# Kernel optimization log

Hardware: AMD Instinct MI355X
Metric: run time of the kernel (lower is better)

The kernel has to match this reference:

```python
import jax, jax.numpy as jnp
import numpy as np

B, S, D, H = 2, 2048, 128, 8  # batch, seq, num_hidden(=head dim), num_heads
EPS = 1e-5


def setup_inputs() -> dict:
    key = jax.random.key(0)
    ks = jax.random.split(key, 12)
    sc = 0.02
    return {
        "query": jax.random.normal(ks[0], (B, S, D), dtype=jnp.float32),
        "Wq": jax.random.normal(ks[1], (2 * H * D, D), dtype=jnp.float32) * sc,
        "bq": jnp.zeros((2 * H * D,), dtype=jnp.float32),
        "Wk": jax.random.normal(ks[2], (2 * H * D, D), dtype=jnp.float32) * sc,
        "bk": jnp.zeros((2 * H * D,), dtype=jnp.float32),
        "Wv": jax.random.normal(ks[3], (H * D, D), dtype=jnp.float32) * sc,
        "bv": jnp.zeros((H * D,), dtype=jnp.float32),
        "Wo": jax.random.normal(ks[4], (D, H * D), dtype=jnp.float32) * sc,
        "bo": jnp.zeros((D,), dtype=jnp.float32),
        "gn_w": jnp.ones((H,), dtype=jnp.float32),
        "gn_b": jnp.zeros((H,), dtype=jnp.float32),
        "lam": jax.random.uniform(ks[5], (), dtype=jnp.float32),
    }


def reference(query, Wq, bq, Wk, bk, Wv, bv, Wo, bo, gn_w, gn_b, lam):
    # Faithful to the torch module: the .view calls are raw reshapes (no
    # transpose), d_k=1 so scale is 1, mask=None path (no causal mask),
    # dropout in eval mode, _lambda == _lambda_init == lam.
    q = (query @ Wq.T + bq).reshape(B, H, S, 2 * D)
    k = (query @ Wk.T + bk).reshape(B, H, S, 2 * D)
    v = (query @ Wv.T + bv).reshape(B, H, S, D)
    q1, q2 = q[..., :D], q[..., D:]
    k1, k2 = k[..., :D], k[..., D:]
    s1 = jnp.einsum("bhqd,bhkd->bhqk", q1, k1)  # / sqrt(d_k=1)
    s2 = jnp.einsum("bhqd,bhkd->bhqk", q2, k2)
    attn = jax.nn.softmax(s1, axis=-1) - lam * jax.nn.softmax(s2, axis=-1)
    out = jnp.einsum("bhqk,bhkd->bhqd", attn, v)          # (B,H,S,D)
    out = out.transpose(0, 2, 1, 3).reshape(B, H, S, D)   # faithful raw reshape
    # GroupNorm(num_groups=H, num_channels=H): normalize per (b, h) over (S, D)
    mean = out.mean(axis=(2, 3), keepdims=True)
    var = out.var(axis=(2, 3), keepdims=True)
    out = (out - mean) * jax.lax.rsqrt(var + EPS)
    out = out * gn_w[None, :, None, None] + gn_b[None, :, None, None]
    out = out * (1.0 - lam)
    # torch.cat([out[:, i] for i in range(H)], dim=-1) -> (B, S, H*D)
    out = out.transpose(0, 2, 1, 3).reshape(B, S, H * D)
    return out @ Wo.T + bo
```

## Files before the change

### kernel.cpp

```cpp
#include <hip/hip_runtime.h>

typedef __bf16 bf16x8 __attribute__((ext_vector_type(8)));
typedef __bf16 bf16x4 __attribute__((ext_vector_type(4)));
typedef float  f32x4  __attribute__((ext_vector_type(4)));

#define MFMA16(a,b,c) __builtin_amdgcn_mfma_f32_16x16x32_bf16((a),(b),(c),0,0,0)

__device__ __forceinline__ bf16x8 cvt8(float4 a, float4 b) {
  bf16x8 v;
  v[0]=(__bf16)a.x; v[1]=(__bf16)a.y; v[2]=(__bf16)a.z; v[3]=(__bf16)a.w;
  v[4]=(__bf16)b.x; v[5]=(__bf16)b.y; v[6]=(__bf16)b.z; v[7]=(__bf16)b.w;
  return v;
}
__device__ __forceinline__ bf16x4 cvt4(float4 a) {
  bf16x4 v;
  v[0]=(__bf16)a.x; v[1]=(__bf16)a.y; v[2]=(__bf16)a.z; v[3]=(__bf16)a.w;
  return v;
}


__global__ void to_bf16(const float* __restrict__ q,  const float* __restrict__ wq,
                        const float* __restrict__ wk, const float* __restrict__ wv,
                        __bf16* __restrict__ qb,  __bf16* __restrict__ wqb,
                        __bf16* __restrict__ wkb, __bf16* __restrict__ wvb)
{
  const long e = (long)(blockIdx.x * 256 + threadIdx.x) * 8;
  const float* src; __bf16* dst; long off;
  if (e < 524288)       { src = q;  dst = qb;  off = e; }
  else if (e < 786432)  { src = wq; dst = wqb; off = e - 524288; }
  else if (e < 1048576) { src = wk; dst = wkb; off = e - 786432; }
  else                  { src = wv; dst = wvb; off = e - 1048576; }
  *(bf16x8*)(dst + off) = cvt8(*(const float4*)(src + off), *(const float4*)(src + off + 4));
}

#define LDA 136
__global__ __launch_bounds__(256, 2) void qkv_gemm(
    const __bf16* __restrict__ queryb,
    const __bf16* __restrict__ Wqb, const float* __restrict__ bq,
    const __bf16* __restrict__ Wkb, const float* __restrict__ bk,
    const __bf16* __restrict__ Wvb, const float* __restrict__ bv,
    __bf16* __restrict__ Qbf, __bf16* __restrict__ Kbf, __bf16* __restrict__ Vbf)
{
  __shared__ __bf16 As[128 * LDA];
  __shared__ __bf16 Bs[128 * LDA];
  const int t = threadIdx.x;
  const int tile = blockIdx.x;
  const int tm = tile / 40, tn = tile % 40;
  const int m0 = tm * 128, n0 = tn * 128;

  const __bf16* wbase; const float* bias;
  __bf16* obase; int ocol0; int ostride; float oscale;
  if (n0 < 2048)      { wbase = Wqb + n0*128;        bias = bq + n0;        obase = Qbf; ocol0 = n0;      ostride = 2048; oscale = 1.4426950408889634f; }
  else if (n0 < 4096) { wbase = Wkb + (n0-2048)*128; bias = bk + (n0-2048); obase = Kbf; ocol0 = n0-2048; ostride = 2048; oscale = 1.0f; }
  else                { wbase = Wvb + (n0-4096)*128; bias = bv + (n0-4096); obase = Vbf; ocol0 = n0-4096; ostride = 1024; oscale = 1.0f; }

  const __bf16* abase = queryb + (long)m0 * 128;
  for (int r = 0; r < 2; ++r) {
    int e = (r*256 + t) * 32;
    int row = e >> 7, col = e & 127;
    #pragma unroll
    for (int c = 0; c < 4; ++c) {
      *(bf16x8*)&As[row*LDA + col + c*8] = *(const bf16x8*)(abase + (long)row*128 + col + c*8);
      *(bf16x8*)&Bs[row*LDA + col + c*8] = *(const bf16x8*)(wbase + (long)row*128 + col + c*8);
    }
  }
  __syncthreads();

  const int w = t >> 6, lane = t & 63;
  const int lo = lane & 15, quad = lane >> 4;
  const int wm = w >> 1, wn = w & 1;

  f32x4 acc[4][4];
  #pragma unroll
  for (int i = 0; i < 4; ++i)
    #pragma unroll
    for (int j = 0; j < 4; ++j) acc[i][j] = (f32x4){0.f,0.f,0.f,0.f};

  #pragma unroll
  for (int ks = 0; ks < 4; ++ks) {
    bf16x8 af[4], bfr[4];
    #pragma unroll
    for (int i = 0; i < 4; ++i)
      af[i] = *(const bf16x8*)&As[(wm*64 + i*16 + lo)*LDA + ks*32 + quad*8];
    #pragma unroll
    for (int j = 0; j < 4; ++j)
      bfr[j] = *(const bf16x8*)&Bs[(wn*64 + j*16 + lo)*LDA + ks*32 + quad*8];
    #pragma unroll
    for (int i = 0; i < 4; ++i)
      #pragma unroll
      for (int j = 0; j < 4; ++j)
        acc[i][j] = MFMA16(bfr[j], af[i], acc[i][j]);
  }
  #pragma unroll
  for (int j = 0; j < 4; ++j) {
    const int colb = ocol0 + wn*64 + j*16 + quad*4;
    const f32x4 b4 = *(const f32x4*)(bias + wn*64 + j*16 + quad*4);
    #pragma unroll
    for (int i = 0; i < 4; ++i) {
      const int row = m0 + wm*64 + i*16 + lo;
      bf16x4 v;
      #pragma unroll
      for (int r = 0; r < 4; ++r) v[r] = (__bf16)((acc[i][j][r] + b4[r]) * oscale);
      *(bf16x4*)&obase[(long)row*ostride + colb] = v;
    }
  }
}

__global__ void v_transpose(const __bf16* __restrict__ Vbf, __bf16* __restrict__ Vt)
{
  __shared__ __bf16 tile[128 * 136];
  const int t = threadIdx.x;
  const int bh = blockIdx.x >> 4, st = blockIdx.x & 15;
  const __bf16* src = Vbf + (long)bh*262144 + st*16384;
  for (int r = 0; r < 8; ++r) {
    int e = (r*256 + t) * 8;
    int row = e >> 7, col = e & 127;
    *(bf16x8*)&tile[row*136 + col] = *(const bf16x8*)(src + row*128 + col);
  }
  __syncthreads();
  __bf16* dst = Vt + (long)bh*262144 + st*128;
  for (int r = 0; r < 8; ++r) {
    int e = (r*256 + t) * 8;
    int d = e >> 7, s2c = e & 127;
    bf16x8 v;
    #pragma unroll
    for (int i = 0; i < 8; ++i) v[i] = tile[(s2c + i)*136 + d];
    *(bf16x8*)(dst + d*2048 + s2c) = v;
  }
}

#define LDK 264
#define LDV 40
__global__ __launch_bounds__(256, 2) void attn(
    const __bf16* __restrict__ Qbf, const __bf16* __restrict__ Kbf,
    const __bf16* __restrict__ Vt, float* __restrict__ O,
    const float* __restrict__ lam_p, float* __restrict__ stats)
{
  __shared__ __bf16 Ks[2][32 * LDK];
  __shared__ __bf16 Vs[2][128 * LDV];
  __shared__ float red[8];
  const int t = threadIdx.x;
  const int w = t >> 6, lane = t & 63;
  const int lo = lane & 15, quad = lane >> 4;
  const int s = w & 1, qg = w >> 1;
  const int bh = blockIdx.x & 15, qb = blockIdx.x >> 4;
  const float lam = *lam_p;

  const __bf16* Qh = Qbf + (long)bh*524288;
  const __bf16* Kh = Kbf + (long)bh*524288;
  const __bf16* Vh = Vt  + (long)bh*262144;
  const int qrow0 = qb*64 + qg*32;

  bf16x8 qf[2][4];
  #pragma unroll
  for (int qt = 0; qt < 2; ++qt)
    #pragma unroll
    for (int ks = 0; ks < 4; ++ks)
      qf[qt][ks] = *(const bf16x8*)(Qh + (long)(qrow0 + qt*16 + lo)*256 + s*128 + ks*32 + quad*8);

  int ke[2], ksrow[2], kcol[2], vdd[2], vch[2];
  #pragma unroll
  for (int r = 0; r < 2; ++r) {
    ke[r] = (r*256 + t) * 16;
    const int row = ke[r] >> 8;
    kcol[r] = ke[r] & 255;
    ksrow[r] = (row & 3) + ((row >> 2) & 1)*16 + ((row >> 3) & 3)*4;
    const int c = r*256 + t;
    vdd[r] = c >> 2; vch[r] = c & 3;
  }

  bf16x8 kra[2][2], vra[2];
  #pragma unroll
  for (int r = 0; r < 2; ++r) {
    kra[r][0] = *(const bf16x8*)(Kh + ke[r]);
    kra[r][1] = *(const bf16x8*)(Kh + ke[r] + 8);
    vra[r]    = *(const bf16x8*)(Vh + (long)vdd[r]*2048 + vch[r]*8);
  }
  #pragma unroll
  for (int r = 0; r < 2; ++r) {
    *(bf16x8*)&Ks[0][ksrow[r]*LDK + kcol[r]]     = kra[r][0];
    *(bf16x8*)&Ks[0][ksrow[r]*LDK + kcol[r] + 8] = kra[r][1];
    *(bf16x8*)&Vs[0][vdd[r]*LDV + vch[r]*8]      = vra[r];
  }

  f32x4 acc[2][8];
  #pragma unroll
  for (int qt = 0; qt < 2; ++qt)
    #pragma unroll
    for (int mt = 0; mt < 8; ++mt) acc[qt][mt] = (f32x4){0.f,0.f,0.f,0.f};
  float lsum[2] = {0.f, 0.f};

  for (int kt = 0; kt < 64; ++kt) {
    __syncthreads();
    if (kt + 1 < 64) {
      #pragma unroll
      for (int r = 0; r < 2; ++r) {
        kra[r][0] = *(const bf16x8*)(Kh + (long)(kt+1)*8192 + ke[r]);
        kra[r][1] = *(const bf16x8*)(Kh + (long)(kt+1)*8192 + ke[r] + 8);
        vra[r]    = *(const bf16x8*)(Vh + (long)vdd[r]*2048 + (kt+1)*32 + vch[r]*8);
      }
    }
    const __bf16* kb = Ks[kt & 1];
    const __bf16* vb = Vs[kt & 1];

    f32x4 sf[2][2];
    #pragma unroll
    for (int qt = 0; qt < 2; ++qt)
      #pragma unroll
      for (int nt = 0; nt < 2; ++nt) sf[qt][nt] = (f32x4){0.f,0.f,0.f,0.f};
    #pragma unroll
    for (int nt = 0; nt < 2; ++nt) {
      const int krow = lo + nt*16;
      #pragma unroll
      for (int ks = 0; ks < 4; ++ks) {
        bf16x8 kf = *(const bf16x8*)&kb[krow*LDK + s*128 + ks*32 + quad*8];
        sf[0][nt] = MFMA16(kf, qf[0][ks], sf[0][nt]);
        sf[1][nt] = MFMA16(kf, qf[1][ks], sf[1][nt]);
      }
    }

    bf16x8 pf[2];
    #pragma unroll
    for (int qt = 0; qt < 2; ++qt) {
      #pragma unroll
      for (int nt = 0; nt < 2; ++nt) {
        #pragma unroll
        for (int r = 0; r < 4; ++r) {
          float p = __builtin_exp2f(sf[qt][nt][r]);
          lsum[qt] += p;
          pf[qt][nt*4+r] = (__bf16)p;
        }
      }
    }

    #pragma unroll
    for (int mt = 0; mt < 8; ++mt) {
      bf16x8 vf = *(const bf16x8*)&vb[(mt*16 + lo)*LDV + quad*8];
      acc[0][mt] = MFMA16(vf, pf[0], acc[0][mt]);
      acc[1][mt] = MFMA16(vf, pf[1], acc[1][mt]);
    }

    if (kt + 1 < 64) {
      __bf16* kn = Ks[(kt+1) & 1];
      __bf16* vn = Vs[(kt+1) & 1];
      #pragma unroll
      for (int r = 0; r < 2; ++r) {
        *(bf16x8*)&kn[ksrow[r]*LDK + kcol[r]]     = kra[r][0];
        *(bf16x8*)&kn[ksrow[r]*LDK + kcol[r] + 8] = kra[r][1];
        *(bf16x8*)&vn[vdd[r]*LDV + vch[r]*8]      = vra[r];
      }
    }
  }

  #pragma unroll
  for (int qt = 0; qt < 2; ++qt) {
    lsum[qt] += __shfl_xor(lsum[qt], 16);
    lsum[qt] += __shfl_xor(lsum[qt], 32);
  }
  float inv[2];
  const float nume = (s == 0) ? 1.f : lam;
  inv[0] = nume / lsum[0];
  inv[1] = nume / lsum[1];

  float* fs = (float*)Ks;
  __syncthreads();
  if (s == 1) {
    #pragma unroll
    for (int qt = 0; qt < 2; ++qt)
      #pragma unroll
      for (int mt = 0; mt < 8; ++mt) {
        f32x4 o;
        #pragma unroll
        for (int r = 0; r < 4; ++r) o[r] = acc[qt][mt][r] * inv[qt];
        *(f32x4*)&fs[(qg*32 + qt*16 + lo)*132 + mt*16 + quad*4] = o;
      }
  }
  __syncthreads();

  float ssum = 0.f, ssq = 0.f;
  if (s == 0) {
    float* Oh = O + (long)bh*262144;
    #pragma unroll
    for (int qt = 0; qt < 2; ++qt)
      #pragma unroll
      for (int mt = 0; mt < 8; ++mt) {
        f32x4 o2 = *(const f32x4*)&fs[(qg*32 + qt*16 + lo)*132 + mt*16 + quad*4];
        f32x4 o;
        #pragma unroll
        for (int r = 0; r < 4; ++r) {
          o[r] = acc[qt][mt][r]*inv[qt] - o2[r];
          ssum += o[r]; ssq += o[r]*o[r];
        }
        *(f32x4*)(Oh + (long)(qrow0 + qt*16 + lo)*128 + mt*16 + quad*4) = o;
      }
  }
  #pragma unroll
  for (int msk = 1; msk < 64; msk <<= 1) { ssum += __shfl_xor(ssum, msk); ssq += __shfl_xor(ssq, msk); }
  if (lane == 0) { red[w] = ssum; red[4 + w] = ssq; }
  __syncthreads();
  if (t == 0) {
    const int g = (bh >> 3)*8 + (qb >> 2);
    atomicAdd(&stats[g*2],   red[0] + red[1] + red[2] + red[3]);
    atomicAdd(&stats[g*2+1], red[4] + red[5] + red[6] + red[7]);
  }
}

#define LDC 72
__global__ __launch_bounds__(256, 2) void out_gemm(
    const float* __restrict__ O, const float* __restrict__ stats,
    const float* __restrict__ gn_w, const float* __restrict__ gn_b,
    const float* __restrict__ lam_p,
    const float* __restrict__ Wo, const float* __restrict__ bo,
    float* __restrict__ out)
{
  __shared__ __bf16 As[64 * LDC];
  __shared__ __bf16 Bs[128 * LDC];
  const int t = threadIdx.x;
  const int w = t >> 6, lane = t & 63;
  const int lo = lane & 15, quad = lane >> 4;
  const int m0 = (blockIdx.x & 63) * 64;
  const int kq = blockIdx.x >> 6;
  const int b = m0 >> 11;
  const float lam1 = 1.f - *lam_p;

  const int hp = kq;
  const float sN   = stats[(b*8 + hp)*2];
  const float ssN  = stats[(b*8 + hp)*2 + 1];
  const float mean = sN * (1.f/262144.f);
  const float rstd = rsqrtf(ssN * (1.f/262144.f) - mean*mean + 1e-5f);
  const float gwv  = gn_w[hp] * rstd * lam1;
  const float shv  = (gn_b[hp] - mean * rstd * gn_w[hp]) * lam1;

  f32x4 acc[8];
  #pragma unroll
  for (int j = 0; j < 8; ++j) acc[j] = (f32x4){0.f,0.f,0.f,0.f};

  for (int kc = 0; kc < 2; ++kc) {
    const int k0 = kq*128 + kc*64;
    const int d0 = kc*64;
    __syncthreads();
    for (int r = 0; r < 4; ++r) {
      int e = r*1024 + t*4;
      int row_l = e >> 6, col_l = e & 63;
      const int spp = (m0 + row_l) & 2047;
      const int h = spp & 7, srow = hp*256 + (spp >> 3);
      float4 v = *(const float4*)(O + ((long)(b*8 + h)*2048 + srow)*128 + d0 + col_l);
      float4 o;
      o.x = v.x*gwv + shv; o.y = v.y*gwv + shv; o.z = v.z*gwv + shv; o.w = v.w*gwv + shv;
      *(bf16x4*)&As[row_l*LDC + col_l] = cvt4(o);
    }
    for (int r = 0; r < 8; ++r) {
      int e = (r*256 + t) * 4;
      int row = e >> 6, col = e & 63;
      *(bf16x4*)&Bs[row*LDC + col] = cvt4(*(const float4*)(Wo + (long)row*1024 + k0 + col));
    }
    __syncthreads();
    #pragma unroll
    for (int ks = 0; ks < 2; ++ks) {
      bf16x8 af = *(const bf16x8*)&As[(w*16 + lo)*LDC + ks*32 + quad*8];
      #pragma unroll
      for (int j = 0; j < 8; ++j) {
        bf16x8 bfr = *(const bf16x8*)&Bs[(j*16 + lo)*LDC + ks*32 + quad*8];
        acc[j] = MFMA16(af, bfr, acc[j]);
      }
    }
  }
  #pragma unroll
  for (int j = 0; j < 8; ++j) {
    const int col = j*16 + lo;
    const float bb = bo[col] * 0.125f;
    #pragma unroll
    for (int r = 0; r < 4; ++r)
      atomicAdd(&out[(long)(m0 + w*16 + quad*4 + r)*128 + col], acc[j][r] + bb);
  }
}

extern "C" void kernel_launch(void* const* d_in, const int* in_sizes, int n_in,
                              void* d_out, int out_size, void* d_ws, size_t ws_size,
                              hipStream_t stream) {
  const float* query = (const float*)d_in[0];
  const float* Wq = (const float*)d_in[1];
  const float* bq = (const float*)d_in[2];
  const float* Wk = (const float*)d_in[3];
  const float* bk = (const float*)d_in[4];
  const float* Wv = (const float*)d_in[5];
  const float* bv = (const float*)d_in[6];
  const float* Wo = (const float*)d_in[7];
  const float* bo = (const float*)d_in[8];
  const float* gn_w = (const float*)d_in[9];
  const float* gn_b = (const float*)d_in[10];
  const float* lam = (const float*)d_in[11];

  char* ws = (char*)d_ws;
  __bf16* Qbf   = (__bf16*)(ws);
  __bf16* Kbf   = (__bf16*)(ws + (16l<<20));
  __bf16* Vbf   = (__bf16*)(ws + (32l<<20));
  __bf16* Vt    = (__bf16*)(ws + (40l<<20));
  float*  O     = (float* )(ws + (48l<<20));
  __bf16* queryb= (__bf16*)(ws + (64l<<20));
  __bf16* Wqb   = (__bf16*)(ws + (65l<<20));
  __bf16* Wkb   = (__bf16*)(ws + (65l<<20) + (512l<<10));
  __bf16* Wvb   = (__bf16*)(ws + (66l<<20));
  float*  stats = (float* )(ws + (66l<<20) + (256l<<10));
  float* out = (float*)d_out;

  to_bf16    <<<dim3(576),  dim3(256), 0, stream>>>(query, Wq, Wk, Wv, queryb, Wqb, Wkb, Wvb);
  qkv_gemm   <<<dim3(1280), dim3(256), 0, stream>>>(queryb, Wqb, bq, Wkb, bk, Wvb, bv, Qbf, Kbf, Vbf);
  v_transpose<<<dim3(256),  dim3(256), 0, stream>>>(Vbf, Vt);
  attn       <<<dim3(512),  dim3(256), 0, stream>>>(Qbf, Kbf, Vt, O, lam, stats);
  out_gemm   <<<dim3(512),  dim3(256), 0, stream>>>(O, stats, gn_w, gn_b, lam, Wo, bo, out);
}
```

Measured before the change: 206.6 us.

## Pre-swizzle K and V into MFMA fragment order and load directly from global

The QKV GEMM epilogue now writes K in a layout matching the attention kernel's MFMA operand fragments, and the V transpose kernel writes V in fragment order too. The attention kernel drops its LDS double-buffered K/V staging and per-iteration barriers, and each lane loads its fragments straight from global memory with contiguous 16-byte accesses. This removes LDS traffic and synchronisation. In exchange, every wave re-reads K/V from global or L2 with no block-level sharing, and global latency is exposed unless enough waves are resident. The K stores in the GEMM epilogue become scattered.

```diff
diff --git a/kernel.cpp b/kernel.cpp
--- a/kernel.cpp
+++ b/kernel.cpp
@@ -49,9 +49,9 @@
   const int m0 = tm * 128, n0 = tn * 128;
 
   const __bf16* wbase; const float* bias;
-  __bf16* obase; int ocol0; int ostride; float oscale;
+  __bf16* obase; int ocol0; int ostride; float oscale; int isK = 0;
   if (n0 < 2048)      { wbase = Wqb + n0*128;        bias = bq + n0;        obase = Qbf; ocol0 = n0;      ostride = 2048; oscale = 1.4426950408889634f; }
-  else if (n0 < 4096) { wbase = Wkb + (n0-2048)*128; bias = bk + (n0-2048); obase = Kbf; ocol0 = n0-2048; ostride = 2048; oscale = 1.0f; }
+  else if (n0 < 4096) { wbase = Wkb + (n0-2048)*128; bias = bk + (n0-2048); obase = Kbf; ocol0 = n0-2048; ostride = 2048; oscale = 1.0f; isK = 1; }
   else                { wbase = Wvb + (n0-4096)*128; bias = bv + (n0-4096); obase = Vbf; ocol0 = n0-4096; ostride = 1024; oscale = 1.0f; }
 
   const __bf16* abase = queryb + (long)m0 * 128;
@@ -101,12 +101,24 @@
       bf16x4 v;
       #pragma unroll
       for (int r = 0; r < 4; ++r) v[r] = (__bf16)((acc[i][j][r] + b4[r]) * oscale);
-      *(bf16x4*)&obase[(long)row*ostride + colb] = v;
-    }
-  }
-}
-
-__global__ void v_transpose(const __bf16* __restrict__ Vbf, __bf16* __restrict__ Vt)
+      if (isK) {
+        const int bh2  = row >> 8;
+        const int key  = ((row & 255) << 3) + (colb >> 8);
+        const int dd0  = colb & 255;
+        const int w5   = key & 31;
+        const int lane2 = (((dd0 >> 3) & 3) << 4) + (((w5 >> 3) << 2) | (w5 & 3));
+        const long flat = (long)bh2 * 524288
+            + ((((long)(key >> 5) * 2 + (dd0 >> 7)) * 4 + ((dd0 >> 5) & 3)) * 2 + ((w5 >> 2) & 1)) * 512
+            + lane2 * 8 + (dd0 & 7);
+        *(bf16x4*)&obase[flat] = v;
+      } else {
+        *(bf16x4*)&obase[(long)row*ostride + colb] = v;
+      }
+    }
+  }
+}
+
+__global__ void v_transpose(const __bf16* __restrict__ Vbf, __bf16* __restrict__ Vfm)
 {
   __shared__ __bf16 tile[128 * 136];
   const int t = threadIdx.x;
@@ -118,27 +130,29 @@
     *(bf16x8*)&tile[row*136 + col] = *(const bf16x8*)(src + row*128 + col);
   }
   __syncthreads();
-  __bf16* dst = Vt + (long)bh*262144 + st*128;
+  __bf16* dst = Vfm + (long)bh*262144 + (long)st*16384;
   for (int r = 0; r < 8; ++r) {
-    int e = (r*256 + t) * 8;
-    int d = e >> 7, s2c = e & 127;
+    const int unit = r*256 + t;
+    const int lane_v = unit & 63;
+    const int m8  = unit >> 6;
+    const int mt  = m8 & 7, ktl = m8 >> 3;
+    const int quad_v = lane_v >> 4, lo_v = lane_v & 15;
     bf16x8 v;
     #pragma unroll
-    for (int i = 0; i < 8; ++i) v[i] = tile[(s2c + i)*136 + d];
-    *(bf16x8*)(dst + d*2048 + s2c) = v;
-  }
-}
-
-#define LDK 264
-#define LDV 40
+    for (int i = 0; i < 8; ++i)
+      v[i] = tile[(ktl*32 + quad_v*8 + i)*136 + mt*16 + lo_v];
+    *(bf16x8*)(dst + (long)ktl*4096 + mt*512 + lane_v*8) = v;
+  }
+}
+
 __global__ __launch_bounds__(256, 2) void attn(
-    const __bf16* __restrict__ Qbf, const __bf16* __restrict__ Kbf,
-    const __bf16* __restrict__ Vt, float* __restrict__ O,
+    const __bf16* __restrict__ Qbf, const __bf16* __restrict__ Kfm,
+    const __bf16* __restrict__ Vfm, float* __restrict__ O,
     const float* __restrict__ lam_p, float* __restrict__ stats)
 {
-  __shared__ __bf16 Ks[2][32 * LDK];
-  __shared__ __bf16 Vs[2][128 * LDV];
-  __shared__ float red[8];
+  __shared__ __align__(16) char pool[33824];
+  float* red = (float*)(pool + 33792);
+
   const int t = threadIdx.x;
   const int w = t >> 6, lane = t & 63;
   const int lo = lane & 15, quad = lane >> 4;
@@ -147,8 +161,8 @@
   const float lam = *lam_p;
 
   const __bf16* Qh = Qbf + (long)bh*524288;
-  const __bf16* Kh = Kbf + (long)bh*524288;
-  const __bf16* Vh = Vt  + (long)bh*262144;
+  const __bf16* Kh = Kfm + (long)bh*524288 + lane*8;
+  const __bf16* Vh = Vfm + (long)bh*262144 + lane*8;
   const int qrow0 = qb*64 + qg*32;
 
   bf16x8 qf[2][4];
@@ -158,31 +172,6 @@
     for (int ks = 0; ks < 4; ++ks)
       qf[qt][ks] = *(const bf16x8*)(Qh + (long)(qrow0 + qt*16 + lo)*256 + s*128 + ks*32 + quad*8);
 
-  int ke[2], ksrow[2], kcol[2], vdd[2], vch[2];
-  #pragma unroll
-  for (int r = 0; r < 2; ++r) {
-    ke[r] = (r*256 + t) * 16;
-    const int row = ke[r] >> 8;
-    kcol[r] = ke[r] & 255;
-    ksrow[r] = (row & 3) + ((row >> 2) & 1)*16 + ((row >> 3) & 3)*4;
-    const int c = r*256 + t;
-    vdd[r] = c >> 2; vch[r] = c & 3;
-  }
-
-  bf16x8 kra[2][2], vra[2];
-  #pragma unroll
-  for (int r = 0; r < 2; ++r) {
-    kra[r][0] = *(const bf16x8*)(Kh + ke[r]);
-    kra[r][1] = *(const bf16x8*)(Kh + ke[r] + 8);
-    vra[r]    = *(const bf16x8*)(Vh + (long)vdd[r]*2048 + vch[r]*8);
-  }
-  #pragma unroll
-  for (int r = 0; r < 2; ++r) {
-    *(bf16x8*)&Ks[0][ksrow[r]*LDK + kcol[r]]     = kra[r][0];
-    *(bf16x8*)&Ks[0][ksrow[r]*LDK + kcol[r] + 8] = kra[r][1];
-    *(bf16x8*)&Vs[0][vdd[r]*LDV + vch[r]*8]      = vra[r];
-  }
-
   f32x4 acc[2][8];
   #pragma unroll
   for (int qt = 0; qt < 2; ++qt)
@@ -191,17 +180,17 @@
   float lsum[2] = {0.f, 0.f};
 
   for (int kt = 0; kt < 64; ++kt) {
-    __syncthreads();
-    if (kt + 1 < 64) {
-      #pragma unroll
-      for (int r = 0; r < 2; ++r) {
-        kra[r][0] = *(const bf16x8*)(Kh + (long)(kt+1)*8192 + ke[r]);
-        kra[r][1] = *(const bf16x8*)(Kh + (long)(kt+1)*8192 + ke[r] + 8);
-        vra[r]    = *(const bf16x8*)(Vh + (long)vdd[r]*2048 + (kt+1)*32 + vch[r]*8);
-      }
-    }
-    const __bf16* kb = Ks[kt & 1];
-    const __bf16* vb = Vs[kt & 1];
+    const __bf16* kp = Kh + (long)(kt*2 + s)*4096;
+    const __bf16* vp = Vh + (long)kt*4096;
+    bf16x8 kf[2][4], vf[8];
+    #pragma unroll
+    for (int ks = 0; ks < 4; ++ks)
+      #pragma unroll
+      for (int nt = 0; nt < 2; ++nt)
+        kf[nt][ks] = *(const bf16x8*)(kp + (ks*2 + nt)*512);
+    #pragma unroll
+    for (int mt = 0; mt < 8; ++mt)
+      vf[mt] = *(const bf16x8*)(vp + mt*512);
 
     f32x4 sf[2][2];
     #pragma unroll
@@ -209,46 +198,29 @@
       #pragma unroll
       for (int nt = 0; nt < 2; ++nt) sf[qt][nt] = (f32x4){0.f,0.f,0.f,0.f};
     #pragma unroll
-    for (int nt = 0; nt < 2; ++nt) {
-      const int krow = lo + nt*16;
+    for (int nt = 0; nt < 2; ++nt)
       #pragma unroll
       for (int ks = 0; ks < 4; ++ks) {
-        bf16x8 kf = *(const bf16x8*)&kb[krow*LDK + s*128 + ks*32 + quad*8];
-        sf[0][nt] = MFMA16(kf, qf[0][ks], sf[0][nt]);
-        sf[1][nt] = MFMA16(kf, qf[1][ks], sf[1][nt]);
-      }
-    }
+        sf[0][nt] = MFMA16(kf[nt][ks], qf[0][ks], sf[0][nt]);
+        sf[1][nt] = MFMA16(kf[nt][ks], qf[1][ks], sf[1][nt]);
+      }
 
     bf16x8 pf[2];
     #pragma unroll
-    for (int qt = 0; qt < 2; ++qt) {
-      #pragma unroll
-      for (int nt = 0; nt < 2; ++nt) {
+    for (int qt = 0; qt < 2; ++qt)
+      #pragma unroll
+      for (int nt = 0; nt < 2; ++nt)
         #pragma unroll
         for (int r = 0; r < 4; ++r) {
           float p = __builtin_exp2f(sf[qt][nt][r]);
           lsum[qt] += p;
           pf[qt][nt*4+r] = (__bf16)p;
         }
-      }
-    }
 
     #pragma unroll
     for (int mt = 0; mt < 8; ++mt) {
-      bf16x8 vf = *(const bf16x8*)&vb[(mt*16 + lo)*LDV + quad*8];
-      acc[0][mt] = MFMA16(vf, pf[0], acc[0][mt]);
-      acc[1][mt] = MFMA16(vf, pf[1], acc[1][mt]);
-    }
-
-    if (kt + 1 < 64) {
-      __bf16* kn = Ks[(kt+1) & 1];
-      __bf16* vn = Vs[(kt+1) & 1];
-      #pragma unroll
-      for (int r = 0; r < 2; ++r) {
-        *(bf16x8*)&kn[ksrow[r]*LDK + kcol[r]]     = kra[r][0];
-        *(bf16x8*)&kn[ksrow[r]*LDK + kcol[r] + 8] = kra[r][1];
-        *(bf16x8*)&vn[vdd[r]*LDV + vch[r]*8]      = vra[r];
-      }
+      acc[0][mt] = MFMA16(vf[mt], pf[0], acc[0][mt]);
+      acc[1][mt] = MFMA16(vf[mt], pf[1], acc[1][mt]);
     }
   }
 
@@ -262,8 +234,7 @@
   inv[0] = nume / lsum[0];
   inv[1] = nume / lsum[1];
 
-  float* fs = (float*)Ks;
-  __syncthreads();
+  float* fs = (float*)pool;
   if (s == 1) {
     #pragma unroll
     for (int qt = 0; qt < 2; ++qt)
@@ -393,9 +364,9 @@
 
   char* ws = (char*)d_ws;
   __bf16* Qbf   = (__bf16*)(ws);
-  __bf16* Kbf   = (__bf16*)(ws + (16l<<20));
+  __bf16* Kfm   = (__bf16*)(ws + (16l<<20));
   __bf16* Vbf   = (__bf16*)(ws + (32l<<20));
-  __bf16* Vt    = (__bf16*)(ws + (40l<<20));
+  __bf16* Vfm   = (__bf16*)(ws + (40l<<20));
   float*  O     = (float* )(ws + (48l<<20));
   __bf16* queryb= (__bf16*)(ws + (64l<<20));
   __bf16* Wqb   = (__bf16*)(ws + (65l<<20));
@@ -405,8 +376,8 @@
   float* out = (float*)d_out;
 
   to_bf16    <<<dim3(576),  dim3(256), 0, stream>>>(query, Wq, Wk, Wv, queryb, Wqb, Wkb, Wvb);
-  qkv_gemm   <<<dim3(1280), dim3(256), 0, stream>>>(queryb, Wqb, bq, Wkb, bk, Wvb, bv, Qbf, Kbf, Vbf);
-  v_transpose<<<dim3(256),  dim3(256), 0, stream>>>(Vbf, Vt);
-  attn       <<<dim3(512),  dim3(256), 0, stream>>>(Qbf, Kbf, Vt, O, lam, stats);
+  qkv_gemm   <<<dim3(1280), dim3(256), 0, stream>>>(queryb, Wqb, bq, Wkb, bk, Wvb, bv, Qbf, Kfm, Vbf);
+  v_transpose<<<dim3(256),  dim3(256), 0, stream>>>(Vbf, Vfm);
+  attn       <<<dim3(512),  dim3(256), 0, stream>>>(Qbf, Kfm, Vfm, O, lam, stats);
   out_gemm   <<<dim3(512),  dim3(256), 0, stream>>>(O, stats, gn_w, gn_b, lam, Wo, bo, out);
 }
```

New measurement: 236.3 us. 14.4% more time.
